# Optimization experiments

Measured on AMD Instinct MI355X. Metric: run time of the kernel, lower is better.

The kernel has to match this reference:

```python
import jax, jax.numpy as jnp
import numpy as np

NUM_HEADS = 16


def setup_inputs() -> dict:
    key = jax.random.key(0)
    k1, k2, k3, k4, k5 = jax.random.split(key, 5)
    B, N, E = 16, 8, 2048
    H = NUM_HEADS
    D = E // H
    KV = 4096
    return {
        "x": jax.random.normal(k1, (B, N, E), dtype=jnp.float32),
        "past_k": jax.random.normal(k2, (B, H, KV, D), dtype=jnp.float32),
        "past_v": jax.random.normal(k3, (B, H, KV, D), dtype=jnp.float32),
        "W_qkv": jax.random.normal(k4, (3 * E, E), dtype=jnp.float32) * (E ** -0.5),
        "W_out": jax.random.normal(k5, (E, E), dtype=jnp.float32) * (E ** -0.5),
    }


def reference(x, past_k, past_v, W_qkv, W_out):
    B, N, E = x.shape
    H = NUM_HEADS
    D = E // H
    # fused QKV projection: [B, N, 3E]
    qkv = jnp.einsum("bne,fe->bnf", x, W_qkv)
    q, k_new, v_new = jnp.split(qkv, 3, axis=-1)
    # '... n (h d) -> ... h n d'
    to_heads = lambda t: t.reshape(B, N, H, D).swapaxes(1, 2)
    q, k_new, v_new = to_heads(q), to_heads(k_new), to_heads(v_new)
    # KV cache append along seq dim
    k = jnp.concatenate([past_k, k_new], axis=-2)  # [B, H, KV+N, D]
    v = jnp.concatenate([past_v, v_new], axis=-2)
    # SDPA (eval mode -> is_causal=False)
    scale = D ** -0.5
    scores = jnp.einsum("bhqd,bhkd->bhqk", q, k) * scale
    attn = jax.nn.softmax(scores, axis=-1)
    out = jnp.einsum("bhqk,bhkd->bhqd", attn, v)  # [B, H, N, D]
    # '... h n d -> ... n (h d)'
    out = out.swapaxes(1, 2).reshape(B, N, E)
    out = jnp.einsum("bne,fe->bnf", out, W_out)
    return (out, k, v)
```

## Files before the change

kernel.cpp:

```cpp
#include <hip/hip_runtime.h>
#include <cstddef>
#include <cstdint>

#define B_ 16
#define H_ 16
#define NQ 8
#define D_ 128
#define E_ 2048
#define F3 6144
#define KVP 4096
#define KVT 4104
#define SCALE 0.08838834764831843f
#define NCHUNK 8
#define CHUNK 512
#define SUBR 32
#define NSUB 16
#define PARTSZ 1040

template <int BM, int BN>
__global__ __launch_bounds__(256) void gemm_xwt(const float* __restrict__ X,
                                                const float* __restrict__ W,
                                                float* __restrict__ C,
                                                int K, int Fdim) {
  constexpr int BK = 32;
  constexpr int RM = BM / 16;
  constexpr int RN = BN / 16;
  __shared__ float xs[BK][BM + 4];
  __shared__ float wss[BK][BN + 4];
  const int t = threadIdx.x;
  const int tm = t >> 4, tn = t & 15;
  const int m0 = blockIdx.y * BM, f0 = blockIdx.x * BN;
  float acc[RM][RN];
#pragma unroll
  for (int i = 0; i < RM; ++i)
#pragma unroll
    for (int j = 0; j < RN; ++j) acc[i][j] = 0.f;

  for (int kk = 0; kk < K; kk += BK) {
#pragma unroll
    for (int i = 0; i < (BM * BK) / 1024; ++i) {
      int j = t + i * 256;
      int r = j >> 3;
      int c = (j & 7) << 2;
      float4 v = *reinterpret_cast<const float4*>(&X[(size_t)(m0 + r) * K + kk + c]);
      xs[c + 0][r] = v.x; xs[c + 1][r] = v.y; xs[c + 2][r] = v.z; xs[c + 3][r] = v.w;
    }
#pragma unroll
    for (int i = 0; i < (BN * BK) / 1024; ++i) {
      int j = t + i * 256;
      int r = j >> 3;
      int c = (j & 7) << 2;
      float4 v = *reinterpret_cast<const float4*>(&W[(size_t)(f0 + r) * K + kk + c]);
      wss[c + 0][r] = v.x; wss[c + 1][r] = v.y; wss[c + 2][r] = v.z; wss[c + 3][r] = v.w;
    }
    __syncthreads();
#pragma unroll
    for (int k = 0; k < BK; ++k) {
      float xv[RM], wv[RN];
      if constexpr (RM == 4) {
        *reinterpret_cast<float4*>(xv) = *reinterpret_cast<const float4*>(&xs[k][tm * 4]);
      } else {
        *reinterpret_cast<float2*>(xv) = *reinterpret_cast<const float2*>(&xs[k][tm * 2]);
      }
      if constexpr (RN == 4) {
        *reinterpret_cast<float4*>(wv) = *reinterpret_cast<const float4*>(&wss[k][tn * 4]);
      } else {
        *reinterpret_cast<float2*>(wv) = *reinterpret_cast<const float2*>(&wss[k][tn * 2]);
      }
#pragma unroll
      for (int i = 0; i < RM; ++i)
#pragma unroll
        for (int j = 0; j < RN; ++j) acc[i][j] += xv[i] * wv[j];
    }
    __syncthreads();
  }
#pragma unroll
  for (int i = 0; i < RM; ++i) {
    float* cp = &C[(size_t)(m0 + tm * RM + i) * Fdim + f0 + tn * RN];
    if constexpr (RN == 4) {
      float4 v = make_float4(acc[i][0], acc[i][1], acc[i][2], acc[i][3]);
      *reinterpret_cast<float4*>(cp) = v;
    } else {
      float2 v = make_float2(acc[i][0], acc[i][1]);
      *reinterpret_cast<float2*>(cp) = v;
    }
  }
}

__global__ __launch_bounds__(256) void attn_partial(
    const float* __restrict__ past_k, const float* __restrict__ past_v,
    const float* __restrict__ qkv, float* __restrict__ out_k,
    float* __restrict__ out_v, float* __restrict__ part) {
  const int t = threadIdx.x;
  const int c = blockIdx.x, h = blockIdx.y, b = blockIdx.z;
  const int bh = b * H_ + h;

  __shared__ float q_lds[NQ * D_];
  __shared__ float k_lds[SUBR * D_];
  __shared__ float v_lds[SUBR * D_];
  __shared__ float p_lds[SUBR * 12];
  __shared__ float cm_lds[NQ], cs_lds[NQ];
  __shared__ float m_lds[2][NQ], l_lds[2][NQ];

  {
    int n = t >> 5, g = t & 31;
    *reinterpret_cast<float4*>(&q_lds[n * D_ + g * 4]) =
        *reinterpret_cast<const float4*>(&qkv[(size_t)(b * NQ + n) * F3 + h * D_ + g * 4]);
  }
  if (t < NQ) { m_lds[0][t] = -1e30f; l_lds[0][t] = 0.f; }

  const int srow = t & 31, sqi = t >> 5;
  const int qg = t >> 7, dcol = t & 127;
  const int pvq = dcol >> 2, pve = dcol & 3;
  float acc[4] = {0.f, 0.f, 0.f, 0.f};

  const float* gk = past_k + ((size_t)bh * KVP + (size_t)c * CHUNK) * D_;
  const float* gv = past_v + ((size_t)bh * KVP + (size_t)c * CHUNK) * D_;
  float* ok = out_k + ((size_t)bh * KVT + (size_t)c * CHUNK) * D_;
  float* ov = out_v + ((size_t)bh * KVT + (size_t)c * CHUNK) * D_;

  __syncthreads();

  for (int sub = 0; sub < NSUB; ++sub) {
    const int cur = sub & 1, nxt = cur ^ 1;
    const size_t off = (size_t)sub * SUBR * D_;
#pragma unroll
    for (int i = 0; i < 4; ++i) {
      int j = t + i * 256;
      int row = j >> 5, g = j & 31;
      size_t ga = off + (size_t)row * D_ + g * 4;
      float4 kv = *reinterpret_cast<const float4*>(&gk[ga]);
      float4 vv = *reinterpret_cast<const float4*>(&gv[ga]);
      *reinterpret_cast<float4*>(&ok[ga]) = kv;
      *reinterpret_cast<float4*>(&ov[ga]) = vv;
      int gs = (g ^ (row & 7)) << 2;
      *reinterpret_cast<float4*>(&k_lds[row * D_ + gs]) = kv;
      *reinterpret_cast<float4*>(&v_lds[row * D_ + gs]) = vv;
    }
    __syncthreads();
    float s = 0.f;
    {
      const int sw = srow & 7;
      const float4* k4 = reinterpret_cast<const float4*>(k_lds);
      const float4* q4 = reinterpret_cast<const float4*>(&q_lds[sqi * D_]);
#pragma unroll
      for (int g = 0; g < 32; ++g) {
        float4 kv = k4[srow * 32 + (g ^ sw)];
        float4 qv = q4[g];
        s += kv.x * qv.x + kv.y * qv.y + kv.z * qv.z + kv.w * qv.w;
      }
    }
    s *= SCALE;
    float cmax = s;
#pragma unroll
    for (int o = 16; o > 0; o >>= 1) cmax = fmaxf(cmax, __shfl_xor(cmax, o));
    float mo = m_lds[cur][sqi];
    float mn = fmaxf(mo, cmax);
    float p = __expf(s - mn);
    float psum = p;
#pragma unroll
    for (int o = 16; o > 0; o >>= 1) psum += __shfl_xor(psum, o);
    p_lds[srow * 12 + sqi] = p;
    if (srow == 0) { cm_lds[sqi] = cmax; cs_lds[sqi] = psum; }
    __syncthreads();
#pragma unroll
    for (int jq = 0; jq < 4; ++jq) {
      int qi = qg * 4 + jq;
      float mo2 = m_lds[cur][qi];
      float mn2 = fmaxf(mo2, cm_lds[qi]);
      acc[jq] *= __expf(mo2 - mn2);
    }
#pragma unroll
    for (int r = 0; r < SUBR; ++r) {
      float4 p4 = *reinterpret_cast<const float4*>(&p_lds[r * 12 + qg * 4]);
      float vv = v_lds[r * D_ + (((pvq ^ (r & 7)) << 2) | pve)];
      acc[0] += p4.x * vv; acc[1] += p4.y * vv;
      acc[2] += p4.z * vv; acc[3] += p4.w * vv;
    }
    if (t < NQ) {
      float mo2 = m_lds[cur][t];
      float mn2 = fmaxf(mo2, cm_lds[t]);
      l_lds[nxt][t] = l_lds[cur][t] * __expf(mo2 - mn2) + cs_lds[t];
      m_lds[nxt][t] = mn2;
    }
    __syncthreads();
  }
  float* pb = part + ((size_t)bh * NCHUNK + c) * PARTSZ;
  if (t < NQ) { pb[t] = m_lds[0][t]; pb[8 + t] = l_lds[0][t]; }
#pragma unroll
  for (int jq = 0; jq < 4; ++jq)
    pb[16 + (size_t)(qg * 4 + jq) * D_ + dcol] = acc[jq];
}

__global__ __launch_bounds__(256) void attn_combine(
    const float* __restrict__ qkv, const float* __restrict__ part,
    float* __restrict__ out_k, float* __restrict__ out_v,
    float* __restrict__ attn) {
  const int t = threadIdx.x;
  const int h = blockIdx.x, b = blockIdx.y;
  const int bh = b * H_ + h;
  __shared__ float q_lds[NQ * 132];
  __shared__ float kn_lds[NQ * 132];
  __shared__ float vn_lds[NQ * 132];
  __shared__ float p9[NQ * 12];
  __shared__ float m9_lds[NQ], s9_lds[NQ];
  {
    int n = t >> 5, g = t & 31;
    const float* src = &qkv[(size_t)(b * NQ + n) * F3 + h * D_ + g * 4];
    float4 qv = *reinterpret_cast<const float4*>(src);
    float4 kv = *reinterpret_cast<const float4*>(src + E_);
    float4 vv = *reinterpret_cast<const float4*>(src + 2 * E_);
    *reinterpret_cast<float4*>(&q_lds[n * 132 + g * 4]) = qv;
    *reinterpret_cast<float4*>(&kn_lds[n * 132 + g * 4]) = kv;
    *reinterpret_cast<float4*>(&vn_lds[n * 132 + g * 4]) = vv;
    *reinterpret_cast<float4*>(&out_k[((size_t)bh * KVT + KVP + n) * D_ + g * 4]) = kv;
    *reinterpret_cast<float4*>(&out_v[((size_t)bh * KVT + KVP + n) * D_ + g * 4]) = vv;
  }
  __syncthreads();
  if (t < 64) {
    int nq = t >> 3, nk = t & 7;
    float s = 0.f;
#pragma unroll
    for (int g = 0; g < 32; ++g) {
      float4 qv = *reinterpret_cast<const float4*>(&q_lds[nq * 132 + g * 4]);
      float4 kv = *reinterpret_cast<const float4*>(&kn_lds[nk * 132 + g * 4]);
      s += qv.x * kv.x + qv.y * kv.y + qv.z * kv.z + qv.w * kv.w;
    }
    s *= SCALE;
    float mx = s;
#pragma unroll
    for (int o = 4; o > 0; o >>= 1) mx = fmaxf(mx, __shfl_xor(mx, o));
    float p = __expf(s - mx);
    float sm = p;
#pragma unroll
    for (int o = 4; o > 0; o >>= 1) sm += __shfl_xor(sm, o);
    p9[nk * 12 + nq] = p;
    if (nk == 0) { m9_lds[nq] = mx; s9_lds[nq] = sm; }
  }
  __syncthreads();
  const int qg = t >> 7, dcol = t & 127;
  const float* pb = part + (size_t)bh * NCHUNK * PARTSZ;
#pragma unroll
  for (int jq = 0; jq < 4; ++jq) {
    int qi = qg * 4 + jq;
    float M = m9_lds[qi];
#pragma unroll
    for (int c = 0; c < NCHUNK; ++c) M = fmaxf(M, pb[(size_t)c * PARTSZ + qi]);
    float num = 0.f, den = 0.f;
#pragma unroll
    for (int c = 0; c < NCHUNK; ++c) {
      const float* pc = pb + (size_t)c * PARTSZ;
      float w = __expf(pc[qi] - M);
      den += w * pc[8 + qi];
      num += w * pc[16 + (size_t)qi * D_ + dcol];
    }
    float acc9 = 0.f;
#pragma unroll
    for (int r = 0; r < NQ; ++r) acc9 += p9[r * 12 + qi] * vn_lds[r * 132 + dcol];
    float w9 = __expf(m9_lds[qi] - M);
    num += w9 * acc9;
    den += w9 * s9_lds[qi];
    attn[((size_t)(b * NQ + qi)) * E_ + h * D_ + dcol] = num / den;
  }
}

extern "C" void kernel_launch(void* const* d_in, const int* in_sizes, int n_in,
                              void* d_out, int out_size, void* d_ws, size_t ws_size,
                              hipStream_t stream) {
  const float* x      = (const float*)d_in[0];
  const float* past_k = (const float*)d_in[1];
  const float* past_v = (const float*)d_in[2];
  const float* W_qkv  = (const float*)d_in[3];
  const float* W_out  = (const float*)d_in[4];

  float* out   = (float*)d_out;
  float* out_k = out + (size_t)B_ * NQ * E_;
  float* out_v = out_k + (size_t)B_ * H_ * KVT * D_;

  float* ws   = (float*)d_ws;
  float* qkv  = ws;
  float* part = qkv + (size_t)B_ * NQ * F3;
  float* attn = part + (size_t)B_ * H_ * NCHUNK * PARTSZ;

  gemm_xwt<64, 64><<<dim3(F3 / 64, 128 / 64), 256, 0, stream>>>(x, W_qkv, qkv, E_, F3);
  attn_partial<<<dim3(NCHUNK, H_, B_), 256, 0, stream>>>(past_k, past_v, qkv, out_k, out_v, part);
  attn_combine<<<dim3(H_, B_), 256, 0, stream>>>(qkv, part, out_k, out_v, attn);
  gemm_xwt<32, 32><<<dim3(E_ / 32, 128 / 32), 256, 0, stream>>>(attn, W_out, out, E_, E_);
}
```

Before: 627.2 us.

## Split-K both GEMMs with atomics and register-resident QK in attention partial

Both projection GEMMs now split the K dimension four ways across a new grid axis and accumulate with float atomicAdd into buffers zeroed by memsets beforehand. This gives the skinny GEMMs more blocks to fill the GPU. The attention partial kernel keeps Q in registers and computes QK dot products straight from the loaded K rows with a shuffle-transpose reduction, which removes the K LDS staging. It also rewrites PV so each wave handles 8 rows with a 4x4 register tile, then reduces across waves through LDS, and sets a 3-blocks-per-SM launch bound. The costs are atomic contention, extra memsets, nondeterministic summation order and more register pressure.

```diff
diff --git a/kernel.cpp b/kernel.cpp
--- a/kernel.cpp
+++ b/kernel.cpp
@@ -17,7 +17,7 @@
 #define NSUB 16
 #define PARTSZ 1040
 
-template <int BM, int BN>
+template <int BM, int BN, int SPLITK>
 __global__ __launch_bounds__(256) void gemm_xwt(const float* __restrict__ X,
                                                 const float* __restrict__ W,
                                                 float* __restrict__ C,
@@ -30,13 +30,14 @@
   const int t = threadIdx.x;
   const int tm = t >> 4, tn = t & 15;
   const int m0 = blockIdx.y * BM, f0 = blockIdx.x * BN;
+  const int kbeg = blockIdx.z * (K / SPLITK), kend = kbeg + K / SPLITK;
   float acc[RM][RN];
 #pragma unroll
   for (int i = 0; i < RM; ++i)
 #pragma unroll
     for (int j = 0; j < RN; ++j) acc[i][j] = 0.f;
 
-  for (int kk = 0; kk < K; kk += BK) {
+  for (int kk = kbeg; kk < kend; kk += BK) {
 #pragma unroll
     for (int i = 0; i < (BM * BK) / 1024; ++i) {
       int j = t + i * 256;
@@ -77,119 +78,169 @@
 #pragma unroll
   for (int i = 0; i < RM; ++i) {
     float* cp = &C[(size_t)(m0 + tm * RM + i) * Fdim + f0 + tn * RN];
-    if constexpr (RN == 4) {
-      float4 v = make_float4(acc[i][0], acc[i][1], acc[i][2], acc[i][3]);
-      *reinterpret_cast<float4*>(cp) = v;
+    if constexpr (SPLITK == 1) {
+      if constexpr (RN == 4) {
+        *reinterpret_cast<float4*>(cp) = make_float4(acc[i][0], acc[i][1], acc[i][2], acc[i][3]);
+      } else {
+        *reinterpret_cast<float2*>(cp) = make_float2(acc[i][0], acc[i][1]);
+      }
     } else {
-      float2 v = make_float2(acc[i][0], acc[i][1]);
-      *reinterpret_cast<float2*>(cp) = v;
+#pragma unroll
+      for (int j = 0; j < RN; ++j) atomicAdd(cp + j, acc[i][j]);
     }
   }
 }
 
-__global__ __launch_bounds__(256) void attn_partial(
+__global__ __launch_bounds__(256, 3) void attn_partial(
     const float* __restrict__ past_k, const float* __restrict__ past_v,
     const float* __restrict__ qkv, float* __restrict__ out_k,
     float* __restrict__ out_v, float* __restrict__ part) {
   const int t = threadIdx.x;
   const int c = blockIdx.x, h = blockIdx.y, b = blockIdx.z;
   const int bh = b * H_ + h;
-
-  __shared__ float q_lds[NQ * D_];
-  __shared__ float k_lds[SUBR * D_];
+  const int g = t & 31, rg = t >> 5;
+
   __shared__ float v_lds[SUBR * D_];
+  __shared__ float s_lds[SUBR * 9];
   __shared__ float p_lds[SUBR * 12];
   __shared__ float cm_lds[NQ], cs_lds[NQ];
   __shared__ float m_lds[2][NQ], l_lds[2][NQ];
 
-  {
-    int n = t >> 5, g = t & 31;
-    *reinterpret_cast<float4*>(&q_lds[n * D_ + g * 4]) =
-        *reinterpret_cast<const float4*>(&qkv[(size_t)(b * NQ + n) * F3 + h * D_ + g * 4]);
-  }
+  float4 qreg[NQ];
+#pragma unroll
+  for (int qi = 0; qi < NQ; ++qi)
+    qreg[qi] = *reinterpret_cast<const float4*>(
+        &qkv[(size_t)(b * NQ + qi) * F3 + h * D_ + g * 4]);
+
   if (t < NQ) { m_lds[0][t] = -1e30f; l_lds[0][t] = 0.f; }
-
-  const int srow = t & 31, sqi = t >> 5;
-  const int qg = t >> 7, dcol = t & 127;
-  const int pvq = dcol >> 2, pve = dcol & 3;
-  float acc[4] = {0.f, 0.f, 0.f, 0.f};
 
   const float* gk = past_k + ((size_t)bh * KVP + (size_t)c * CHUNK) * D_;
   const float* gv = past_v + ((size_t)bh * KVP + (size_t)c * CHUNK) * D_;
   float* ok = out_k + ((size_t)bh * KVT + (size_t)c * CHUNK) * D_;
   float* ov = out_v + ((size_t)bh * KVT + (size_t)c * CHUNK) * D_;
 
+  const int w = t >> 6;
+  const int lqg = (t >> 5) & 1;
+  const int dq = t & 31;
+  float acc[4][4];
+#pragma unroll
+  for (int i = 0; i < 4; ++i)
+#pragma unroll
+    for (int j = 0; j < 4; ++j) acc[i][j] = 0.f;
+
+  const int b0 = g & 1, b1 = (g >> 1) & 1, b2 = (g >> 2) & 1;
+  const int qsel = 4 * b0 + 2 * b1 + b2;
+
   __syncthreads();
 
   for (int sub = 0; sub < NSUB; ++sub) {
     const int cur = sub & 1, nxt = cur ^ 1;
     const size_t off = (size_t)sub * SUBR * D_;
+
+    float4 kf[4], vf[4];
 #pragma unroll
     for (int i = 0; i < 4; ++i) {
-      int j = t + i * 256;
-      int row = j >> 5, g = j & 31;
-      size_t ga = off + (size_t)row * D_ + g * 4;
-      float4 kv = *reinterpret_cast<const float4*>(&gk[ga]);
-      float4 vv = *reinterpret_cast<const float4*>(&gv[ga]);
-      *reinterpret_cast<float4*>(&ok[ga]) = kv;
-      *reinterpret_cast<float4*>(&ov[ga]) = vv;
-      int gs = (g ^ (row & 7)) << 2;
-      *reinterpret_cast<float4*>(&k_lds[row * D_ + gs]) = kv;
-      *reinterpret_cast<float4*>(&v_lds[row * D_ + gs]) = vv;
-    }
-    __syncthreads();
-    float s = 0.f;
+      const size_t ga = off + (size_t)(rg + 8 * i) * D_ + g * 4;
+      kf[i] = *reinterpret_cast<const float4*>(&gk[ga]);
+      vf[i] = *reinterpret_cast<const float4*>(&gv[ga]);
+    }
+#pragma unroll
+    for (int i = 0; i < 4; ++i) {
+      const int r = rg + 8 * i;
+      const size_t ga = off + (size_t)r * D_ + g * 4;
+      *reinterpret_cast<float4*>(&ok[ga]) = kf[i];
+      *reinterpret_cast<float4*>(&ov[ga]) = vf[i];
+      *reinterpret_cast<float4*>(&v_lds[r * D_ + g * 4]) = vf[i];
+      float sp[NQ];
+#pragma unroll
+      for (int qi = 0; qi < NQ; ++qi)
+        sp[qi] = kf[i].x * qreg[qi].x + kf[i].y * qreg[qi].y +
+                 kf[i].z * qreg[qi].z + kf[i].w * qreg[qi].w;
+      float v1[4];
+#pragma unroll
+      for (int j = 0; j < 4; ++j) {
+        float x = b0 ? sp[j] : sp[j + 4];
+        v1[j] = (b0 ? sp[j + 4] : sp[j]) + __shfl_xor(x, 1);
+      }
+      float v2[2];
+#pragma unroll
+      for (int j = 0; j < 2; ++j) {
+        float x = b1 ? v1[j] : v1[j + 2];
+        v2[j] = (b1 ? v1[j + 2] : v1[j]) + __shfl_xor(x, 2);
+      }
+      float v3;
+      {
+        float x = b2 ? v2[0] : v2[1];
+        v3 = (b2 ? v2[1] : v2[0]) + __shfl_xor(x, 4);
+      }
+      v3 += __shfl_xor(v3, 8);
+      v3 += __shfl_xor(v3, 16);
+      if (g < 8) s_lds[r * 9 + qsel] = v3;
+    }
+    __syncthreads();
+
     {
-      const int sw = srow & 7;
-      const float4* k4 = reinterpret_cast<const float4*>(k_lds);
-      const float4* q4 = reinterpret_cast<const float4*>(&q_lds[sqi * D_]);
-#pragma unroll
-      for (int g = 0; g < 32; ++g) {
-        float4 kv = k4[srow * 32 + (g ^ sw)];
-        float4 qv = q4[g];
-        s += kv.x * qv.x + kv.y * qv.y + kv.z * qv.z + kv.w * qv.w;
-      }
-    }
-    s *= SCALE;
-    float cmax = s;
-#pragma unroll
-    for (int o = 16; o > 0; o >>= 1) cmax = fmaxf(cmax, __shfl_xor(cmax, o));
-    float mo = m_lds[cur][sqi];
-    float mn = fmaxf(mo, cmax);
-    float p = __expf(s - mn);
-    float psum = p;
-#pragma unroll
-    for (int o = 16; o > 0; o >>= 1) psum += __shfl_xor(psum, o);
-    p_lds[srow * 12 + sqi] = p;
-    if (srow == 0) { cm_lds[sqi] = cmax; cs_lds[sqi] = psum; }
-    __syncthreads();
-#pragma unroll
-    for (int jq = 0; jq < 4; ++jq) {
-      int qi = qg * 4 + jq;
-      float mo2 = m_lds[cur][qi];
-      float mn2 = fmaxf(mo2, cm_lds[qi]);
-      acc[jq] *= __expf(mo2 - mn2);
-    }
-#pragma unroll
-    for (int r = 0; r < SUBR; ++r) {
-      float4 p4 = *reinterpret_cast<const float4*>(&p_lds[r * 12 + qg * 4]);
-      float vv = v_lds[r * D_ + (((pvq ^ (r & 7)) << 2) | pve)];
-      acc[0] += p4.x * vv; acc[1] += p4.y * vv;
-      acc[2] += p4.z * vv; acc[3] += p4.w * vv;
-    }
-    if (t < NQ) {
-      float mo2 = m_lds[cur][t];
-      float mn2 = fmaxf(mo2, cm_lds[t]);
-      l_lds[nxt][t] = l_lds[cur][t] * __expf(mo2 - mn2) + cs_lds[t];
-      m_lds[nxt][t] = mn2;
-    }
-    __syncthreads();
-  }
+      const int srow = t & 31, sqi = t >> 5;
+      float s = s_lds[srow * 9 + sqi] * SCALE;
+      float cmax = s;
+#pragma unroll
+      for (int o = 16; o > 0; o >>= 1) cmax = fmaxf(cmax, __shfl_xor(cmax, o));
+      float mo = m_lds[cur][sqi];
+      float mn = fmaxf(mo, cmax);
+      float p = __expf(s - mn);
+      float psum = p;
+#pragma unroll
+      for (int o = 16; o > 0; o >>= 1) psum += __shfl_xor(psum, o);
+      p_lds[srow * 12 + sqi] = p;
+      if (srow == 0) { cm_lds[sqi] = cmax; cs_lds[sqi] = psum; }
+    }
+    __syncthreads();
+
+    {
+#pragma unroll
+      for (int jq = 0; jq < 4; ++jq) {
+        const int qi = lqg * 4 + jq;
+        float mo = m_lds[cur][qi];
+        float f = __expf(mo - fmaxf(mo, cm_lds[qi]));
+        acc[jq][0] *= f; acc[jq][1] *= f; acc[jq][2] *= f; acc[jq][3] *= f;
+      }
+#pragma unroll
+      for (int r8 = 0; r8 < 8; ++r8) {
+        const int r = w * 8 + r8;
+        float4 p4 = *reinterpret_cast<const float4*>(&p_lds[r * 12 + lqg * 4]);
+        float4 v4 = *reinterpret_cast<const float4*>(&v_lds[r * D_ + dq * 4]);
+        acc[0][0] += p4.x * v4.x; acc[0][1] += p4.x * v4.y; acc[0][2] += p4.x * v4.z; acc[0][3] += p4.x * v4.w;
+        acc[1][0] += p4.y * v4.x; acc[1][1] += p4.y * v4.y; acc[1][2] += p4.y * v4.z; acc[1][3] += p4.y * v4.w;
+        acc[2][0] += p4.z * v4.x; acc[2][1] += p4.z * v4.y; acc[2][2] += p4.z * v4.z; acc[2][3] += p4.z * v4.w;
+        acc[3][0] += p4.w * v4.x; acc[3][1] += p4.w * v4.y; acc[3][2] += p4.w * v4.z; acc[3][3] += p4.w * v4.w;
+      }
+      if (t < NQ) {
+        float mo = m_lds[cur][t];
+        float mn = fmaxf(mo, cm_lds[t]);
+        l_lds[nxt][t] = l_lds[cur][t] * __expf(mo - mn) + cs_lds[t];
+        m_lds[nxt][t] = mn;
+      }
+    }
+    __syncthreads();
+  }
+
+#pragma unroll
+  for (int jq = 0; jq < 4; ++jq)
+    *reinterpret_cast<float4*>(&v_lds[w * 1024 + (lqg * 4 + jq) * D_ + dq * 4]) =
+        make_float4(acc[jq][0], acc[jq][1], acc[jq][2], acc[jq][3]);
+  __syncthreads();
+
   float* pb = part + ((size_t)bh * NCHUNK + c) * PARTSZ;
   if (t < NQ) { pb[t] = m_lds[0][t]; pb[8 + t] = l_lds[0][t]; }
-#pragma unroll
-  for (int jq = 0; jq < 4; ++jq)
-    pb[16 + (size_t)(qg * 4 + jq) * D_ + dcol] = acc[jq];
+  {
+    float4 s0 = *reinterpret_cast<const float4*>(&v_lds[t * 4]);
+    float4 s1 = *reinterpret_cast<const float4*>(&v_lds[1024 + t * 4]);
+    float4 s2 = *reinterpret_cast<const float4*>(&v_lds[2048 + t * 4]);
+    float4 s3 = *reinterpret_cast<const float4*>(&v_lds[3072 + t * 4]);
+    float4 r4 = make_float4(s0.x + s1.x + s2.x + s3.x, s0.y + s1.y + s2.y + s3.y,
+                            s0.z + s1.z + s2.z + s3.z, s0.w + s1.w + s2.w + s3.w);
+    *reinterpret_cast<float4*>(&pb[16 + t * 4]) = r4;
+  }
 }
 
 __global__ __launch_bounds__(256) void attn_combine(
@@ -250,9 +301,9 @@
 #pragma unroll
     for (int c = 0; c < NCHUNK; ++c) {
       const float* pc = pb + (size_t)c * PARTSZ;
-      float w = __expf(pc[qi] - M);
-      den += w * pc[8 + qi];
-      num += w * pc[16 + (size_t)qi * D_ + dcol];
+      float wgt = __expf(pc[qi] - M);
+      den += wgt * pc[8 + qi];
+      num += wgt * pc[16 + (size_t)qi * D_ + dcol];
     }
     float acc9 = 0.f;
 #pragma unroll
@@ -282,8 +333,11 @@
   float* part = qkv + (size_t)B_ * NQ * F3;
   float* attn = part + (size_t)B_ * H_ * NCHUNK * PARTSZ;
 
-  gemm_xwt<64, 64><<<dim3(F3 / 64, 128 / 64), 256, 0, stream>>>(x, W_qkv, qkv, E_, F3);
+  hipMemsetAsync(qkv, 0, (size_t)B_ * NQ * F3 * sizeof(float), stream);
+  hipMemsetAsync(out, 0, (size_t)B_ * NQ * E_ * sizeof(float), stream);
+
+  gemm_xwt<64, 64, 4><<<dim3(F3 / 64, 128 / 64, 4), 256, 0, stream>>>(x, W_qkv, qkv, E_, F3);
   attn_partial<<<dim3(NCHUNK, H_, B_), 256, 0, stream>>>(past_k, past_v, qkv, out_k, out_v, part);
   attn_combine<<<dim3(H_, B_), 256, 0, stream>>>(qkv, part, out_k, out_v, attn);
-  gemm_xwt<32, 32><<<dim3(E_ / 32, 128 / 32), 256, 0, stream>>>(attn, W_out, out, E_, E_);
+  gemm_xwt<32, 32, 4><<<dim3(E_ / 32, 128 / 32, 4), 256, 0, stream>>>(attn, W_out, out, E_, E_);
 }
```

Result: slower. 676.2 us (+7.8%).
